# Optimization experiments

Measured on AMD Instinct MI355X. Metric: run time of the kernel, lower is better.

The kernel has to match this reference:

```python
import jax, jax.numpy as jnp
import numpy as np
import math

B, L, D, K = 8, 8192, 256, 2
J = math.ceil(math.log((L - 1) / (K - 1) + 1) / math.log(K))  # 13 for L=8192, K=2


def setup_inputs() -> dict:
    key = jax.random.key(0)
    kx, k0, k1, kw = jax.random.split(key, 4)
    # matches nn.initializers.normal(stddev=h_scale) in the flax module
    h_scale = math.sqrt((math.gamma(K / 2) / math.gamma(J + K / 2)) ** (1.0 / J) / 2.0)
    x = jax.random.normal(kx, (B, L, D), dtype=jnp.float32)
    h0 = jax.random.normal(k0, (D, K), dtype=jnp.float32) * h_scale
    h1 = jax.random.normal(k1, (D, K), dtype=jnp.float32) * h_scale
    w = jax.random.normal(kw, (J + 2, D), dtype=jnp.float32) / math.sqrt(J + 2)
    return {"x": x, "h0": h0, "h1": h1, "w": w}


def _depthwise_conv(a, filt, dilation, d):
    # a: (B, L', D), filt: (1, D, K) in IOL layout, depthwise via feature_group_count=D
    return jax.lax.conv_general_dilated(
        lhs=a, rhs=filt, window_strides=(1,), padding='VALID',
        dimension_numbers=('NLC', 'IOL', 'NLC'),
        rhs_dilation=(dilation,), feature_group_count=d)


def reference(x, h0, h1, w):
    Kf = h0.shape[-1]
    Dd = x.shape[-1]
    h0r = h0[None, :, :]  # (1, D, K)
    h1r = h1[None, :, :]
    Jlv = w.shape[0] - 2
    y = jnp.zeros_like(x)
    a = x
    for j in range(Jlv):
        dilation = Kf ** j
        pad = dilation * (Kf - 1)
        a = jnp.pad(a, ((0, 0), (pad, 0), (0, 0)))  # pad left (pad_right=False)
        b = _depthwise_conv(a, h1r, dilation, Dd)
        a = _depthwise_conv(a, h0r, dilation, Dd)
        y = y + w[j + 1][None, None, :] * b
    y = y + w[None, :1, :] * x + w[None, -1:, :] * a
    return y
```

## Files before the change

kernel.cpp:

```cpp
#include <hip/hip_runtime.h>
#include <hip/hip_bf16.h>
#include <stdint.h>

namespace {

constexpr int L = 8192;
constexpr int D = 256;

constexpr int K1_CT  = 32;
constexpr int K1_OUT = 192;
constexpr int K1_S   = 265;

constexpr int K2_CT = 32;
constexpr int K2_T2 = 2;
constexpr int K2_S  = 131;

__device__ __forceinline__ int phi1(int p) { return p + (p >> 5); }
__device__ __forceinline__ int phi2(int t) { return t + (t >> 5); }

__device__ __forceinline__ uint32_t pk2(float ylo, float ahi) {
    union { __hip_bfloat16 h; uint16_t u; } a, b;
    a.h = __float2bfloat16(ylo);
    b.h = __float2bfloat16(ahi);
    return ((uint32_t)b.u << 16) | (uint32_t)a.u;
}
__device__ __forceinline__ float up_lo(uint32_t u) { return __uint_as_float(u << 16); }
__device__ __forceinline__ float up_hi(uint32_t u) { return __uint_as_float(u & 0xffff0000u); }

__device__ __forceinline__ void lvl4(float (&a)[4], float (&y)[4],
                                     float l0, float l1, float l2, float l3,
                                     float h00, float h01, float h10, float h11,
                                     float wj) {
    const float lk[4] = {l0, l1, l2, l3};
#pragma unroll
    for (int i = 0; i < 4; ++i) {
        const float bv = lk[i] * h10 + a[i] * h11;
        y[i] = fmaf(wj, bv, y[i]);
        a[i] = lk[i] * h00 + a[i] * h01;
    }
}

__device__ __forceinline__ void lvl2f(float& a0, float& a1, float& y0, float& y1,
                                      float l0, float l1,
                                      float h00, float h01, float h10, float h11,
                                      float wj) {
    const float bv0 = l0 * h10 + a0 * h11;
    const float bv1 = l1 * h10 + a1 * h11;
    y0 = fmaf(wj, bv0, y0);
    y1 = fmaf(wj, bv1, y1);
    a0 = l0 * h00 + a0 * h01;
    a1 = l1 * h00 + a1 * h01;
}

__global__ __launch_bounds__(256, 4)
void mrl_k1(const float* __restrict__ x, const float* __restrict__ h0,
            const float* __restrict__ h1, const float* __restrict__ w,
            uint32_t* __restrict__ out_pk) {
    __shared__ uint32_t lds[K1_CT * K1_S];
    const int tid = threadIdx.x;
    const int b  = blockIdx.z;
    const int c0 = blockIdx.y * K1_CT;
    const int t0 = blockIdx.x * K1_OUT;
    const int tsb = t0 - 64;

    {
        const int cq = (tid & 7) * 4;
        const int tr = tid >> 3;
        const float* xb = x + (size_t)b * L * D + c0 + cq;
#pragma unroll
        for (int it = 0; it < 8; ++it) {
            const int p = it * 32 + tr;
            const int t = tsb + p;
            float4 v = make_float4(0.f, 0.f, 0.f, 0.f);
            if (t >= 0 && t < L) v = *reinterpret_cast<const float4*>(xb + (size_t)t * D);
            const int ph = phi1(p);
            lds[(cq + 0) * K1_S + ph] = __float_as_uint(v.x);
            lds[(cq + 1) * K1_S + ph] = __float_as_uint(v.y);
            lds[(cq + 2) * K1_S + ph] = __float_as_uint(v.z);
            lds[(cq + 3) * K1_S + ph] = __float_as_uint(v.w);
        }
    }
    __syncthreads();

    {
        const int lane = tid & 63;
        const int wv   = tid >> 6;
        const int p0   = 4 * lane;
#pragma unroll
        for (int q = 0; q < 8; ++q) {
            const int cl = wv + 4 * q;
            const int c  = c0 + cl;
            const float h00 = h0[2*c], h01 = h0[2*c+1];
            const float h10 = h1[2*c], h11 = h1[2*c+1];
            const int base = cl * K1_S;
            float a[4], y[4];
            {
                const float w0 = w[c];
#pragma unroll
                for (int i = 0; i < 4; ++i) {
                    a[i] = __uint_as_float(lds[base + phi1(p0 + i)]);
                    y[i] = w0 * a[i];
                }
            }
            lvl4(a, y, __shfl_up(a[3], 1), a[0], a[1], a[2],
                 h00, h01, h10, h11, w[1*D + c]);
            lvl4(a, y, __shfl_up(a[2], 1), __shfl_up(a[3], 1), a[0], a[1],
                 h00, h01, h10, h11, w[2*D + c]);
            lvl4(a, y, __shfl_up(a[0], 1), __shfl_up(a[1], 1),
                       __shfl_up(a[2], 1), __shfl_up(a[3], 1),
                 h00, h01, h10, h11, w[3*D + c]);
            lvl4(a, y, __shfl_up(a[0], 2), __shfl_up(a[1], 2),
                       __shfl_up(a[2], 2), __shfl_up(a[3], 2),
                 h00, h01, h10, h11, w[4*D + c]);
            lvl4(a, y, __shfl_up(a[0], 4), __shfl_up(a[1], 4),
                       __shfl_up(a[2], 4), __shfl_up(a[3], 4),
                 h00, h01, h10, h11, w[5*D + c]);
            lvl4(a, y, __shfl_up(a[0], 8), __shfl_up(a[1], 8),
                       __shfl_up(a[2], 8), __shfl_up(a[3], 8),
                 h00, h01, h10, h11, w[6*D + c]);
#pragma unroll
            for (int i = 0; i < 4; ++i)
                lds[base + phi1(p0 + i)] = pk2(y[i], a[i]);
        }
    }
    __syncthreads();

    {
        const int cq = (tid & 7) * 4;
        const int tr = tid >> 3;
        uint32_t* ob = out_pk + (size_t)b * L * D + c0 + cq;
#pragma unroll
        for (int it = 0; it < 6; ++it) {
            const int p = 64 + it * 32 + tr;
            const int t = tsb + p;
            if (t < L) {
                const int ph = phi1(p);
                uint4 v;
                v.x = lds[(cq + 0) * K1_S + ph];
                v.y = lds[(cq + 1) * K1_S + ph];
                v.z = lds[(cq + 2) * K1_S + ph];
                v.w = lds[(cq + 3) * K1_S + ph];
                *reinterpret_cast<uint4*>(ob + (size_t)t * D) = v;
            }
        }
    }
}

__global__ __launch_bounds__(256, 4)
void mrl_k2(const float* __restrict__ h0, const float* __restrict__ h1,
            const float* __restrict__ w, float* __restrict__ y) {
    __shared__ uint32_t lds[K2_CT * K2_T2 * K2_S];
    const int tid = threadIdx.x;
    const int b   = blockIdx.z;
    const int c0  = blockIdx.y * K2_CT;
    const int t2a = blockIdx.x * K2_T2;
    uint32_t* yb = reinterpret_cast<uint32_t*>(y) + (size_t)b * L * D + c0;

    {
        const int cq  = (tid & 7) * 4;
        const int t2i = (tid >> 3) & 1;
        const int t1r = tid >> 4;
#pragma unroll
        for (int it = 0; it < 8; ++it) {
            const int t1 = it * 16 + t1r;
            const int t  = t1 * 64 + t2a + t2i;
            const uint4 v = *reinterpret_cast<const uint4*>(yb + (size_t)t * D + cq);
            const int ph = phi2(t1);
            lds[((cq + 0) * 2 + t2i) * K2_S + ph] = v.x;
            lds[((cq + 1) * 2 + t2i) * K2_S + ph] = v.y;
            lds[((cq + 2) * 2 + t2i) * K2_S + ph] = v.z;
            lds[((cq + 3) * 2 + t2i) * K2_S + ph] = v.w;
        }
    }
    __syncthreads();

    {
        const int lane = tid & 63;
        const int wv   = tid >> 6;
#pragma unroll
        for (int q = 0; q < 16; ++q) {
            const int pr = wv + 4 * q;
            const int c  = c0 + (pr >> 1);
            const float h00 = h0[2*c], h01 = h0[2*c+1];
            const float h10 = h1[2*c], h11 = h1[2*c+1];
            const int base = pr * K2_S;
            float a0, a1, y0, y1v;
            {
                const uint32_t u0 = lds[base + phi2(2 * lane)];
                const uint32_t u1 = lds[base + phi2(2 * lane + 1)];
                a0 = up_hi(u0); y0  = up_lo(u0);
                a1 = up_hi(u1); y1v = up_lo(u1);
            }
            {
                const float s = __shfl_up(a1, 1);
                const float l0 = (lane >= 1) ? s : 0.f;
                lvl2f(a0, a1, y0, y1v, l0, a0, h00, h01, h10, h11, w[7*D + c]);
            }
#pragma unroll
            for (int k = 0; k < 6; ++k) {
                const int m = 1 << k;
                const float wj = w[(8 + k) * D + c];
                const float s0 = __shfl_up(a0, m);
                const float s1 = __shfl_up(a1, m);
                const bool ok = (lane >= m);
                const float l0 = ok ? s0 : 0.f;
                const float l1 = ok ? s1 : 0.f;
                lvl2f(a0, a1, y0, y1v, l0, l1, h00, h01, h10, h11, wj);
            }
            const float w14 = w[14*D + c];
            y0  = fmaf(w14, a0, y0);
            y1v = fmaf(w14, a1, y1v);
            lds[base + phi2(2 * lane)]     = __float_as_uint(y0);
            lds[base + phi2(2 * lane + 1)] = __float_as_uint(y1v);
        }
    }
    __syncthreads();

    {
        const int cq = (tid & 7) * 4;
        const int rq = tid >> 3;
#pragma unroll
        for (int it = 0; it < 8; ++it) {
            const int row = it * 32 + rq;
            const int t1 = row >> 1, t2i = row & 1;
            const int t  = t1 * 64 + t2a + t2i;
            const int ph = phi2(t1);
            uint4 v;
            v.x = lds[((cq + 0) * 2 + t2i) * K2_S + ph];
            v.y = lds[((cq + 1) * 2 + t2i) * K2_S + ph];
            v.z = lds[((cq + 2) * 2 + t2i) * K2_S + ph];
            v.w = lds[((cq + 3) * 2 + t2i) * K2_S + ph];
            *reinterpret_cast<uint4*>(yb + (size_t)t * D + cq) = v;
        }
    }
}

}

extern "C" void kernel_launch(void* const* d_in, const int* in_sizes, int n_in,
                              void* d_out, int out_size, void* d_ws, size_t ws_size,
                              hipStream_t stream) {
    const float* x  = (const float*)d_in[0];
    const float* h0 = (const float*)d_in[1];
    const float* h1 = (const float*)d_in[2];
    const float* w  = (const float*)d_in[3];
    float* y = (float*)d_out;
    (void)d_ws; (void)ws_size;

    const int B = in_sizes[0] / (L * D);

    dim3 g1((L + K1_OUT - 1) / K1_OUT, D / K1_CT, B);
    dim3 g2(64 / K2_T2, D / K2_CT, B);

    mrl_k1<<<g1, 256, 0, stream>>>(x, h0, h1, w, (uint32_t*)y);
    mrl_k2<<<g2, 256, 0, stream>>>(h0, h1, w, y);
}
```

Measured before the change: 174.2 us.

## Switch scan math to packed fp16 pairs and double block size

```diff
diff --git a/kernel.cpp b/kernel.cpp
--- a/kernel.cpp
+++ b/kernel.cpp
@@ -1,5 +1,5 @@
 #include <hip/hip_runtime.h>
-#include <hip/hip_bf16.h>
+#include <hip/hip_fp16.h>
 #include <stdint.h>
 
 namespace {
@@ -9,50 +9,50 @@
 
 constexpr int K1_CT  = 32;
 constexpr int K1_OUT = 192;
-constexpr int K1_S   = 265;
+constexpr int K1_S   = 270;
 
 constexpr int K2_CT = 32;
 constexpr int K2_T2 = 2;
-constexpr int K2_S  = 131;
-
-__device__ __forceinline__ int phi1(int p) { return p + (p >> 5); }
-__device__ __forceinline__ int phi2(int t) { return t + (t >> 5); }
-
-__device__ __forceinline__ uint32_t pk2(float ylo, float ahi) {
-    union { __hip_bfloat16 h; uint16_t u; } a, b;
-    a.h = __float2bfloat16(ylo);
-    b.h = __float2bfloat16(ahi);
-    return ((uint32_t)b.u << 16) | (uint32_t)a.u;
-}
-__device__ __forceinline__ float up_lo(uint32_t u) { return __uint_as_float(u << 16); }
-__device__ __forceinline__ float up_hi(uint32_t u) { return __uint_as_float(u & 0xffff0000u); }
-
-__device__ __forceinline__ void lvl4(float (&a)[4], float (&y)[4],
-                                     float l0, float l1, float l2, float l3,
-                                     float h00, float h01, float h10, float h11,
-                                     float wj) {
-    const float lk[4] = {l0, l1, l2, l3};
+constexpr int K2_S  = 134;
+
+__device__ __forceinline__ int phie(int p) { return p + 2 * (p >> 5); }
+
+__device__ __forceinline__ uint32_t h2u(__half2 v) { return __builtin_bit_cast(uint32_t, v); }
+__device__ __forceinline__ __half2 u2h(uint32_t v) { return __builtin_bit_cast(__half2, v); }
+
+__device__ __forceinline__ __half2 h2up(__half2 v, int m) {
+    return u2h((uint32_t)__shfl_up((int)h2u(v), m));
+}
+__device__ __forceinline__ __half2 h2upz(__half2 v, int m, int lane) {
+    const int s = __shfl_up((int)h2u(v), m);
+    return u2h((lane >= m) ? (uint32_t)s : 0u);
+}
+
+__device__ __forceinline__ void plvl4(__half2 (&A)[4], __half2 (&Y)[4],
+                                      const __half2 (&lk)[4],
+                                      __half2 c00, __half2 c01, __half2 c10,
+                                      __half2 c11, __half2 wj) {
 #pragma unroll
     for (int i = 0; i < 4; ++i) {
-        const float bv = lk[i] * h10 + a[i] * h11;
-        y[i] = fmaf(wj, bv, y[i]);
-        a[i] = lk[i] * h00 + a[i] * h01;
-    }
-}
-
-__device__ __forceinline__ void lvl2f(float& a0, float& a1, float& y0, float& y1,
-                                      float l0, float l1,
-                                      float h00, float h01, float h10, float h11,
-                                      float wj) {
-    const float bv0 = l0 * h10 + a0 * h11;
-    const float bv1 = l1 * h10 + a1 * h11;
-    y0 = fmaf(wj, bv0, y0);
-    y1 = fmaf(wj, bv1, y1);
-    a0 = l0 * h00 + a0 * h01;
-    a1 = l1 * h00 + a1 * h01;
-}
-
-__global__ __launch_bounds__(256, 4)
+        const __half2 bv = __hfma2(A[i], c11, __hmul2(lk[i], c10));
+        Y[i] = __hfma2(wj, bv, Y[i]);
+        A[i] = __hfma2(A[i], c01, __hmul2(lk[i], c00));
+    }
+}
+
+__device__ __forceinline__ void plvl2(__half2& A0, __half2& A1, __half2& Y0, __half2& Y1,
+                                      __half2 l0, __half2 l1,
+                                      __half2 c00, __half2 c01, __half2 c10,
+                                      __half2 c11, __half2 wj) {
+    const __half2 bv0 = __hfma2(A0, c11, __hmul2(l0, c10));
+    const __half2 bv1 = __hfma2(A1, c11, __hmul2(l1, c10));
+    Y0 = __hfma2(wj, bv0, Y0);
+    Y1 = __hfma2(wj, bv1, Y1);
+    A0 = __hfma2(A0, c01, __hmul2(l0, c00));
+    A1 = __hfma2(A1, c01, __hmul2(l1, c00));
+}
+
+__global__ __launch_bounds__(512, 8)
 void mrl_k1(const float* __restrict__ x, const float* __restrict__ h0,
             const float* __restrict__ h1, const float* __restrict__ w,
             uint32_t* __restrict__ out_pk) {
@@ -64,20 +64,28 @@
     const int tsb = t0 - 64;
 
     {
-        const int cq = (tid & 7) * 4;
-        const int tr = tid >> 3;
-        const float* xb = x + (size_t)b * L * D + c0 + cq;
-#pragma unroll
-        for (int it = 0; it < 8; ++it) {
-            const int p = it * 32 + tr;
-            const int t = tsb + p;
-            float4 v = make_float4(0.f, 0.f, 0.f, 0.f);
-            if (t >= 0 && t < L) v = *reinterpret_cast<const float4*>(xb + (size_t)t * D);
-            const int ph = phi1(p);
-            lds[(cq + 0) * K1_S + ph] = __float_as_uint(v.x);
-            lds[(cq + 1) * K1_S + ph] = __float_as_uint(v.y);
-            lds[(cq + 2) * K1_S + ph] = __float_as_uint(v.z);
-            lds[(cq + 3) * K1_S + ph] = __float_as_uint(v.w);
+        const float* xb = x + (size_t)b * L * D + c0;
+#pragma unroll
+        for (int it = 0; it < 2; ++it) {
+            const int tau = tid + 512 * it;
+            const int cq = (tau & 7) * 4;
+            const int pr = tau >> 3;
+            const int t = tsb + 2 * pr;
+            float4 v0 = make_float4(0.f, 0.f, 0.f, 0.f);
+            float4 v1 = v0;
+            if (t >= 0 && t < L)
+                v0 = *reinterpret_cast<const float4*>(xb + (size_t)t * D + cq);
+            if (t + 1 >= 0 && t + 1 < L)
+                v1 = *reinterpret_cast<const float4*>(xb + (size_t)(t + 1) * D + cq);
+            const int ph = phie(2 * pr);
+            uint2 p0 = make_uint2(__float_as_uint(v0.x), __float_as_uint(v1.x));
+            uint2 p1 = make_uint2(__float_as_uint(v0.y), __float_as_uint(v1.y));
+            uint2 p2 = make_uint2(__float_as_uint(v0.z), __float_as_uint(v1.z));
+            uint2 p3 = make_uint2(__float_as_uint(v0.w), __float_as_uint(v1.w));
+            *reinterpret_cast<uint2*>(&lds[(cq + 0) * K1_S + ph]) = p0;
+            *reinterpret_cast<uint2*>(&lds[(cq + 1) * K1_S + ph]) = p1;
+            *reinterpret_cast<uint2*>(&lds[(cq + 2) * K1_S + ph]) = p2;
+            *reinterpret_cast<uint2*>(&lds[(cq + 3) * K1_S + ph]) = p3;
         }
     }
     __syncthreads();
@@ -85,42 +93,69 @@
     {
         const int lane = tid & 63;
         const int wv   = tid >> 6;
-        const int p0   = 4 * lane;
-#pragma unroll
-        for (int q = 0; q < 8; ++q) {
-            const int cl = wv + 4 * q;
-            const int c  = c0 + cl;
-            const float h00 = h0[2*c], h01 = h0[2*c+1];
-            const float h10 = h1[2*c], h11 = h1[2*c+1];
-            const int base = cl * K1_S;
-            float a[4], y[4];
-            {
-                const float w0 = w[c];
-#pragma unroll
-                for (int i = 0; i < 4; ++i) {
-                    a[i] = __uint_as_float(lds[base + phi1(p0 + i)]);
-                    y[i] = w0 * a[i];
-                }
+        const int p0i  = 4 * lane;
+        const int ph0  = phie(p0i);
+
+#pragma unroll
+        for (int u = 0; u < 2; ++u) {
+            const int rA = wv + 16 * u;
+            const int rB = rA + 8;
+            const int cA = __builtin_amdgcn_readfirstlane(c0 + rA);
+            const int cB = __builtin_amdgcn_readfirstlane(c0 + rB);
+            const __half2 c00 = __floats2half2_rn(h0[2*cA],   h0[2*cB]);
+            const __half2 c01 = __floats2half2_rn(h0[2*cA+1], h0[2*cB+1]);
+            const __half2 c10 = __floats2half2_rn(h1[2*cA],   h1[2*cB]);
+            const __half2 c11 = __floats2half2_rn(h1[2*cA+1], h1[2*cB+1]);
+            const __half2 w0v = __floats2half2_rn(w[cA], w[cB]);
+            __half2 wj[6];
+#pragma unroll
+            for (int j = 0; j < 6; ++j)
+                wj[j] = __floats2half2_rn(w[(j+1)*D + cA], w[(j+1)*D + cB]);
+
+            const uint32_t* pa = &lds[rA * K1_S + ph0];
+            const uint32_t* pb = &lds[rB * K1_S + ph0];
+            const uint2 ra0 = *reinterpret_cast<const uint2*>(pa);
+            const uint2 ra1 = *reinterpret_cast<const uint2*>(pa + 2);
+            const uint2 rb0 = *reinterpret_cast<const uint2*>(pb);
+            const uint2 rb1 = *reinterpret_cast<const uint2*>(pb + 2);
+            __half2 A[4], Y[4], lk[4];
+            A[0] = __floats2half2_rn(__uint_as_float(ra0.x), __uint_as_float(rb0.x));
+            A[1] = __floats2half2_rn(__uint_as_float(ra0.y), __uint_as_float(rb0.y));
+            A[2] = __floats2half2_rn(__uint_as_float(ra1.x), __uint_as_float(rb1.x));
+            A[3] = __floats2half2_rn(__uint_as_float(ra1.y), __uint_as_float(rb1.y));
+#pragma unroll
+            for (int i = 0; i < 4; ++i) Y[i] = __hmul2(w0v, A[i]);
+
+            lk[0] = h2up(A[3], 1); lk[1] = A[0]; lk[2] = A[1]; lk[3] = A[2];
+            plvl4(A, Y, lk, c00, c01, c10, c11, wj[0]);
+            lk[0] = h2up(A[2], 1); lk[1] = h2up(A[3], 1); lk[2] = A[0]; lk[3] = A[1];
+            plvl4(A, Y, lk, c00, c01, c10, c11, wj[1]);
+            lk[0] = h2up(A[0], 1); lk[1] = h2up(A[1], 1);
+            lk[2] = h2up(A[2], 1); lk[3] = h2up(A[3], 1);
+            plvl4(A, Y, lk, c00, c01, c10, c11, wj[2]);
+            lk[0] = h2up(A[0], 2); lk[1] = h2up(A[1], 2);
+            lk[2] = h2up(A[2], 2); lk[3] = h2up(A[3], 2);
+            plvl4(A, Y, lk, c00, c01, c10, c11, wj[3]);
+            lk[0] = h2up(A[0], 4); lk[1] = h2up(A[1], 4);
+            lk[2] = h2up(A[2], 4); lk[3] = h2up(A[3], 4);
+            plvl4(A, Y, lk, c00, c01, c10, c11, wj[4]);
+            lk[0] = h2up(A[0], 8); lk[1] = h2up(A[1], 8);
+            lk[2] = h2up(A[2], 8); lk[3] = h2up(A[3], 8);
+            plvl4(A, Y, lk, c00, c01, c10, c11, wj[5]);
+
+            uint32_t wA[4], wB[4];
+#pragma unroll
+            for (int i = 0; i < 4; ++i) {
+                const uint32_t Au = h2u(A[i]), Yu = h2u(Y[i]);
+                wA[i] = (Yu & 0xffffu) | (Au << 16);
+                wB[i] = (Yu >> 16)     | (Au & 0xffff0000u);
             }
-            lvl4(a, y, __shfl_up(a[3], 1), a[0], a[1], a[2],
-                 h00, h01, h10, h11, w[1*D + c]);
-            lvl4(a, y, __shfl_up(a[2], 1), __shfl_up(a[3], 1), a[0], a[1],
-                 h00, h01, h10, h11, w[2*D + c]);
-            lvl4(a, y, __shfl_up(a[0], 1), __shfl_up(a[1], 1),
-                       __shfl_up(a[2], 1), __shfl_up(a[3], 1),
-                 h00, h01, h10, h11, w[3*D + c]);
-            lvl4(a, y, __shfl_up(a[0], 2), __shfl_up(a[1], 2),
-                       __shfl_up(a[2], 2), __shfl_up(a[3], 2),
-                 h00, h01, h10, h11, w[4*D + c]);
-            lvl4(a, y, __shfl_up(a[0], 4), __shfl_up(a[1], 4),
-                       __shfl_up(a[2], 4), __shfl_up(a[3], 4),
-                 h00, h01, h10, h11, w[5*D + c]);
-            lvl4(a, y, __shfl_up(a[0], 8), __shfl_up(a[1], 8),
-                       __shfl_up(a[2], 8), __shfl_up(a[3], 8),
-                 h00, h01, h10, h11, w[6*D + c]);
-#pragma unroll
-            for (int i = 0; i < 4; ++i)
-                lds[base + phi1(p0 + i)] = pk2(y[i], a[i]);
+            uint32_t* qa = &lds[rA * K1_S + ph0];
+            uint32_t* qb = &lds[rB * K1_S + ph0];
+            *reinterpret_cast<uint2*>(qa)     = make_uint2(wA[0], wA[1]);
+            *reinterpret_cast<uint2*>(qa + 2) = make_uint2(wA[2], wA[3]);
+            *reinterpret_cast<uint2*>(qb)     = make_uint2(wB[0], wB[1]);
+            *reinterpret_cast<uint2*>(qb + 2) = make_uint2(wB[2], wB[3]);
         }
     }
     __syncthreads();
@@ -130,11 +165,11 @@
         const int tr = tid >> 3;
         uint32_t* ob = out_pk + (size_t)b * L * D + c0 + cq;
 #pragma unroll
-        for (int it = 0; it < 6; ++it) {
-            const int p = 64 + it * 32 + tr;
+        for (int it = 0; it < 3; ++it) {
+            const int p = 64 + it * 64 + tr;
             const int t = tsb + p;
             if (t < L) {
-                const int ph = phi1(p);
+                const int ph = phie(p);
                 uint4 v;
                 v.x = lds[(cq + 0) * K1_S + ph];
                 v.y = lds[(cq + 1) * K1_S + ph];
@@ -146,7 +181,7 @@
     }
 }
 
-__global__ __launch_bounds__(256, 4)
+__global__ __launch_bounds__(512, 8)
 void mrl_k2(const float* __restrict__ h0, const float* __restrict__ h1,
             const float* __restrict__ w, float* __restrict__ y) {
     __shared__ uint32_t lds[K2_CT * K2_T2 * K2_S];
@@ -157,19 +192,21 @@
     uint32_t* yb = reinterpret_cast<uint32_t*>(y) + (size_t)b * L * D + c0;
 
     {
-        const int cq  = (tid & 7) * 4;
-        const int t2i = (tid >> 3) & 1;
-        const int t1r = tid >> 4;
-#pragma unroll
-        for (int it = 0; it < 8; ++it) {
-            const int t1 = it * 16 + t1r;
-            const int t  = t1 * 64 + t2a + t2i;
-            const uint4 v = *reinterpret_cast<const uint4*>(yb + (size_t)t * D + cq);
-            const int ph = phi2(t1);
-            lds[((cq + 0) * 2 + t2i) * K2_S + ph] = v.x;
-            lds[((cq + 1) * 2 + t2i) * K2_S + ph] = v.y;
-            lds[((cq + 2) * 2 + t2i) * K2_S + ph] = v.z;
-            lds[((cq + 3) * 2 + t2i) * K2_S + ph] = v.w;
+#pragma unroll
+        for (int it = 0; it < 2; ++it) {
+            const int tau = tid + 512 * it;
+            const int cq  = (tau & 7) * 4;
+            const int t2i = (tau >> 3) & 1;
+            const int u   = tau >> 4;
+            const uint4 v0 = *reinterpret_cast<const uint4*>(
+                yb + (size_t)((2*u)   * 64 + t2a + t2i) * D + cq);
+            const uint4 v1 = *reinterpret_cast<const uint4*>(
+                yb + (size_t)((2*u+1) * 64 + t2a + t2i) * D + cq);
+            const int ph = phie(2 * u);
+            *reinterpret_cast<uint2*>(&lds[((cq + 0) * 2 + t2i) * K2_S + ph]) = make_uint2(v0.x, v1.x);
+            *reinterpret_cast<uint2*>(&lds[((cq + 1) * 2 + t2i) * K2_S + ph]) = make_uint2(v0.y, v1.y);
+            *reinterpret_cast<uint2*>(&lds[((cq + 2) * 2 + t2i) * K2_S + ph]) = make_uint2(v0.z, v1.z);
+            *reinterpret_cast<uint2*>(&lds[((cq + 3) * 2 + t2i) * K2_S + ph]) = make_uint2(v0.w, v1.w);
         }
     }
     __syncthreads();
@@ -177,41 +214,54 @@
     {
         const int lane = tid & 63;
         const int wv   = tid >> 6;
-#pragma unroll
-        for (int q = 0; q < 16; ++q) {
-            const int pr = wv + 4 * q;
-            const int c  = c0 + (pr >> 1);
-            const float h00 = h0[2*c], h01 = h0[2*c+1];
-            const float h10 = h1[2*c], h11 = h1[2*c+1];
-            const int base = pr * K2_S;
-            float a0, a1, y0, y1v;
+        const int ph0  = phie(2 * lane);
+
+#pragma unroll
+        for (int q = 0; q < 4; ++q) {
+            const int rowA = wv + 8 * q;
+            const int cA = __builtin_amdgcn_readfirstlane(c0 + (rowA >> 1));
+            const int cB = cA + 16;
+            const __half2 c00 = __floats2half2_rn(h0[2*cA],   h0[2*cB]);
+            const __half2 c01 = __floats2half2_rn(h0[2*cA+1], h0[2*cB+1]);
+            const __half2 c10 = __floats2half2_rn(h1[2*cA],   h1[2*cB]);
+            const __half2 c11 = __floats2half2_rn(h1[2*cA+1], h1[2*cB+1]);
+            __half2 wj[7];
+#pragma unroll
+            for (int j = 0; j < 7; ++j)
+                wj[j] = __floats2half2_rn(w[(7+j)*D + cA], w[(7+j)*D + cB]);
+            const __half2 w14v = __floats2half2_rn(w[14*D + cA], w[14*D + cB]);
+
+            uint32_t* pa = &lds[rowA * K2_S + ph0];
+            uint32_t* pb = &lds[(rowA + 32) * K2_S + ph0];
+            const uint2 wa = *reinterpret_cast<const uint2*>(pa);
+            const uint2 wb = *reinterpret_cast<const uint2*>(pb);
+            __half2 A0 = u2h((wa.x >> 16) | (wb.x & 0xffff0000u));
+            __half2 Y0 = u2h((wa.x & 0xffffu) | (wb.x << 16));
+            __half2 A1 = u2h((wa.y >> 16) | (wb.y & 0xffff0000u));
+            __half2 Y1 = u2h((wa.y & 0xffffu) | (wb.y << 16));
+
             {
-                const uint32_t u0 = lds[base + phi2(2 * lane)];
-                const uint32_t u1 = lds[base + phi2(2 * lane + 1)];
-                a0 = up_hi(u0); y0  = up_lo(u0);
-                a1 = up_hi(u1); y1v = up_lo(u1);
-            }
-            {
-                const float s = __shfl_up(a1, 1);
-                const float l0 = (lane >= 1) ? s : 0.f;
-                lvl2f(a0, a1, y0, y1v, l0, a0, h00, h01, h10, h11, w[7*D + c]);
+                const __half2 l0 = h2upz(A1, 1, lane);
+                const __half2 l1 = A0;
+                plvl2(A0, A1, Y0, Y1, l0, l1, c00, c01, c10, c11, wj[0]);
             }
 #pragma unroll
             for (int k = 0; k < 6; ++k) {
                 const int m = 1 << k;
-                const float wj = w[(8 + k) * D + c];
-                const float s0 = __shfl_up(a0, m);
-                const float s1 = __shfl_up(a1, m);
-                const bool ok = (lane >= m);
-                const float l0 = ok ? s0 : 0.f;
-                const float l1 = ok ? s1 : 0.f;
-                lvl2f(a0, a1, y0, y1v, l0, l1, h00, h01, h10, h11, wj);
+                const __half2 l0 = h2upz(A0, m, lane);
+                const __half2 l1 = h2upz(A1, m, lane);
+                plvl2(A0, A1, Y0, Y1, l0, l1, c00, c01, c10, c11, wj[1 + k]);
             }
-            const float w14 = w[14*D + c];
-            y0  = fmaf(w14, a0, y0);
-            y1v = fmaf(w14, a1, y1v);
-            lds[base + phi2(2 * lane)]     = __float_as_uint(y0);
-            lds[base + phi2(2 * lane + 1)] = __float_as_uint(y1v);
+            Y0 = __hfma2(w14v, A0, Y0);
+            Y1 = __hfma2(w14v, A1, Y1);
+
+            uint2 oa, ob;
+            oa.x = __float_as_uint(__low2float(Y0));
+            oa.y = __float_as_uint(__low2float(Y1));
+            ob.x = __float_as_uint(__high2float(Y0));
+            ob.y = __float_as_uint(__high2float(Y1));
+            *reinterpret_cast<uint2*>(pa) = oa;
+            *reinterpret_cast<uint2*>(pb) = ob;
         }
     }
     __syncthreads();
@@ -220,11 +270,11 @@
         const int cq = (tid & 7) * 4;
         const int rq = tid >> 3;
 #pragma unroll
-        for (int it = 0; it < 8; ++it) {
-            const int row = it * 32 + rq;
+        for (int it = 0; it < 4; ++it) {
+            const int row = it * 64 + rq;
             const int t1 = row >> 1, t2i = row & 1;
             const int t  = t1 * 64 + t2a + t2i;
-            const int ph = phi2(t1);
+            const int ph = phie(t1);
             uint4 v;
             v.x = lds[((cq + 0) * 2 + t2i) * K2_S + ph];
             v.y = lds[((cq + 1) * 2 + t2i) * K2_S + ph];
@@ -252,6 +302,6 @@
     dim3 g1((L + K1_OUT - 1) / K1_OUT, D / K1_CT, B);
     dim3 g2(64 / K2_T2, D / K2_CT, B);
 
-    mrl_k1<<<g1, 256, 0, stream>>>(x, h0, h1, w, (uint32_t*)y);
-    mrl_k2<<<g2, 256, 0, stream>>>(h0, h1, w, y);
-}
+    mrl_k1<<<g1, 512, 0, stream>>>(x, h0, h1, w, (uint32_t*)y);
+    mrl_k2<<<g2, 512, 0, stream>>>(h0, h1, w, y);
+}
```

New measurement: 152.6 us. 12.4% less time.
